# Kernel tuning notes

Hardware: AMD Instinct MI355X
Metric: run time of the kernel (lower is better)

Reference implementation:

```python
import jax, jax.numpy as jnp
import numpy as np
from jax import lax

B = 1024
T = 32           # length_sec = 384 // (2*2*3*1)
HGT = 7          # height_image = 28 // (1*2*2*1)
CC = 32          # last conv channels
AD = HGT * CC    # abstract_dim = 224
HID = 256        # attention decoder hidden
VOCAB = 29
OUT_LEN = 25


def setup_inputs() -> dict:
    ks = jax.random.split(jax.random.key(0), 24)
    n = lambda k, s, sc=1.0: jax.random.normal(k, s, jnp.float32) * sc
    return {
        "x": n(ks[0], (B, 1, 384, 28)),
        "conv1_w": n(ks[1], (4, 1, 3, 3), 0.2),   "conv1_b": n(ks[2], (4,), 0.1),
        "conv2_w": n(ks[3], (16, 4, 3, 3), 0.2),  "conv2_b": n(ks[4], (16,), 0.1),
        "conv3_w": n(ks[5], (16, 16, 3, 3), 0.2), "conv3_b": n(ks[6], (16,), 0.1),
        "conv4_w": n(ks[7], (32, 16, 3, 3), 0.2), "conv4_b": n(ks[8], (32,), 0.1),
        "h0": n(ks[9], (1, AD)), "c0": n(ks[10], (1, AD)),
        "lstm_Wih": n(ks[11], (4 * AD, AD), 0.05), "lstm_Whh": n(ks[12], (4 * AD, AD), 0.05),
        "lstm_bih": n(ks[13], (4 * AD,), 0.05),    "lstm_bhh": n(ks[14], (4 * AD,), 0.05),
        "att_w": n(ks[15], (1, HID + AD), 0.05),   "att_b": n(ks[16], (1,), 0.05),
        "dec_Wih": n(ks[17], (4 * HID, AD), 0.05), "dec_Whh": n(ks[18], (4 * HID, HID), 0.05),
        "dec_bih": n(ks[19], (4 * HID,), 0.05),    "dec_bhh": n(ks[20], (4 * HID,), 0.05),
        "out_w": n(ks[21], (VOCAB, HID), 0.05),    "out_b": n(ks[22], (VOCAB,), 0.05),
    }


def _lstm_cell(h, c, xt, Wih, Whh, bih, bhh):
    # PyTorch gate order: i, f, g, o
    g = xt @ Wih.T + bih + h @ Whh.T + bhh
    i, f, gg, o = jnp.split(g, 4, axis=-1)
    c = jax.nn.sigmoid(f) * c + jax.nn.sigmoid(i) * jnp.tanh(gg)
    h = jax.nn.sigmoid(o) * jnp.tanh(c)
    return h, c


def reference(x, conv1_w, conv1_b, conv2_w, conv2_b, conv3_w, conv3_b, conv4_w, conv4_b,
              h0, c0, lstm_Wih, lstm_Whh, lstm_bih, lstm_bhh,
              att_w, att_b, dec_Wih, dec_Whh, dec_bih, dec_bhh, out_w, out_b):
    def crp(z, w, b, pool):
        y = lax.conv_general_dilated(z, w, (1, 1), [(1, 1), (1, 1)],
                                     dimension_numbers=('NCHW', 'OIHW', 'NCHW'))
        y = jax.nn.relu(y + b[None, :, None, None])
        win = (1, 1) + pool
        return lax.reduce_window(y, -jnp.inf, lax.max, win, win, 'VALID')

    y1 = crp(x, conv1_w, conv1_b, (2, 1))
    y2 = crp(y1, conv2_w, conv2_b, (2, 2))
    y3 = crp(y2, conv3_w, conv3_b, (3, 2))
    y4 = crp(y3, conv4_w, conv4_b, (1, 1))          # [B, 32, 32, 7]
    Bsz = x.shape[0]
    # y5[b,t,i] = y4[b, i%32, t, i//32]  ==  transpose + reshape (replaces python loop)
    y5 = jnp.transpose(y4, (0, 2, 3, 1)).reshape(Bsz, T, AD)   # [B, T, 224]

    # encoder LSTM (seq-major scan, like torch LSTM)
    def estep(carry, xt):
        h, c = carry
        h, c = _lstm_cell(h, c, xt, lstm_Wih, lstm_Whh, lstm_bih, lstm_bhh)
        return (h, c), h
    h0b = jnp.tile(h0, (Bsz, 1))
    c0b = jnp.tile(c0, (Bsz, 1))
    _, hs = lax.scan(estep, (h0b, c0b), jnp.transpose(y5, (1, 0, 2)))
    y8 = jnp.transpose(hs, (1, 0, 2))                # [B, T, 224]

    # attention decoder: additive score softmax(linear(concat(h, enc)))
    w_h = att_w[0, :HID]     # hidden part
    w_e = att_w[0, HID:]     # encoder part
    enc_score = y8 @ w_e     # [B, T], precomputed once

    def dstep(carry, _):
        h, c = carry
        scores = enc_score + (h @ w_h)[:, None] + att_b[0]      # [B, T]
        alpha = jax.nn.softmax(scores, axis=1)
        ctx = jnp.einsum('bt,btd->bd', alpha, y8)               # [B, 224]
        h, c = _lstm_cell(h, c, ctx, dec_Wih, dec_Whh, dec_bih, dec_bhh)
        return (h, c), h @ out_w.T + out_b                      # [B, 29]

    hdec = jnp.zeros((Bsz, HID), x.dtype)
    _, outs = lax.scan(dstep, (hdec, hdec), None, length=OUT_LEN)  # [25, B, 29]
    return jnp.transpose(outs, (1, 2, 0))            # [B, 29, 25]
```

## Files before the change

kernel.cpp:

```cpp
#include <hip/hip_runtime.h>

typedef unsigned short u16;
typedef unsigned int u32;
typedef unsigned long long u64;
typedef __bf16 bfrag __attribute__((ext_vector_type(8)));
typedef float v4f __attribute__((ext_vector_type(4)));

#define DI __device__ __forceinline__

DI float bf2f(u16 b){ union{u32 u; float f;} c; c.u = ((u32)b)<<16; return c.f; }
DI u16 f2bf(float f){ union{float f; u32 u;} c; c.f=f; u32 u=c.u; return (u16)((u + 0x7FFFu + ((u>>16)&1u))>>16); }
DI float sigm(float x){ return 1.0f/(1.0f+__expf(-x)); }
DI float tanhf_(float x){ float a=fabsf(x); float e=__expf(2.0f*a); float r=1.0f-2.0f/(e+1.0f); return x<0.0f? -r : r; }

__global__ __launch_bounds__(256) void k_cvt2(const float* __restrict__ src, u16* __restrict__ hi,
                                              u16* __restrict__ lo, u32 n){
  u32 i = blockIdx.x*256u + threadIdx.x;
  if (i < n){ float v = src[i]; u16 h = f2bf(v); hi[i] = h; lo[i] = f2bf(v - bf2f(h)); }
}

__global__ __launch_bounds__(256) void k_conv1(const float* __restrict__ x, const float* __restrict__ w,
                                               const float* __restrict__ bias, float* __restrict__ y1q, u32 bbase){
  u32 gid = blockIdx.x*256u + threadIdx.x;
  u32 bl = gid/768u, r = gid - bl*768u;
  u32 oy = r>>2, xg = r&3u;
  const float* xb = x + (u64)(bbase+bl)*10752u;
  float win[4][9];
  #pragma unroll
  for (int rr=0; rr<4; rr++){
    int iy = 2*(int)oy - 1 + rr;
    bool vy = (u32)iy < 384u;
    #pragma unroll
    for (int cc=0; cc<9; cc++){
      int ix = (int)(xg*7u) + cc - 1;
      win[rr][cc] = (vy && (u32)ix < 28u) ? xb[iy*28 + ix] : 0.0f;
    }
  }
  #pragma unroll
  for (int co=0; co<4; co++){
    float wf[9];
    #pragma unroll
    for (int j=0;j<9;j++) wf[j] = w[co*9+j];
    float bc = bias[co];
    float* outp = y1q + ((u64)(bl*4u+co)*192u + oy)*28u + xg*7u;
    #pragma unroll
    for (int ox=0; ox<7; ox++){
      float m = 0.0f;
      #pragma unroll
      for (int py=0; py<2; py++){
        float s = bc;
        #pragma unroll
        for (int dy=0; dy<3; dy++)
          #pragma unroll
          for (int dx=0; dx<3; dx++)
            s += win[py+dy][ox+dx]*wf[dy*3+dx];
        m = fmaxf(m, s);
      }
      outp[ox] = m;
    }
  }
}

__global__ __launch_bounds__(256) void k_conv2(const float* __restrict__ y1q, const float* __restrict__ w,
                                               const float* __restrict__ bias, float* __restrict__ y2q){
  u32 gid = blockIdx.x*256u + threadIdx.x;
  u32 bl = gid/1536u, r = gid - bl*1536u;
  u32 oy = r>>4, xg = (r>>3)&1u, cp = r&7u;
  const float* inb = y1q + (u64)bl*21504u;
  float acc[2][7][4];
  #pragma unroll
  for (int c2=0;c2<2;c2++)
    #pragma unroll
    for (int i=0;i<7;i++){ acc[c2][i][0]=0.f;acc[c2][i][1]=0.f;acc[c2][i][2]=0.f;acc[c2][i][3]=0.f; }
  for (int ci=0; ci<4; ci++){
    float win[4][16];
    const float* pl = inb + ci*5376;
    #pragma unroll
    for (int rr=0; rr<4; rr++){
      int iy = 2*(int)oy - 1 + rr;
      bool vy = (u32)iy < 192u;
      #pragma unroll
      for (int cc=0; cc<16; cc++){
        int ix = (int)(xg*14u) + cc - 1;
        win[rr][cc] = (vy && (u32)ix<28u) ? pl[iy*28+ix] : 0.0f;
      }
    }
    float wf[2][9];
    #pragma unroll
    for (int c2=0;c2<2;c2++)
      #pragma unroll
      for (int j=0;j<9;j++) wf[c2][j] = w[((cp*2u+(u32)c2)*4u+(u32)ci)*9u+j];
    #pragma unroll
    for (int c2=0;c2<2;c2++)
      #pragma unroll
      for (int ol=0; ol<7; ol++)
        #pragma unroll
        for (int py=0; py<2; py++)
          #pragma unroll
          for (int px=0; px<2; px++){
            float s = acc[c2][ol][py*2+px];
            #pragma unroll
            for (int dy=0; dy<3; dy++)
              #pragma unroll
              for (int dx=0; dx<3; dx++)
                s += win[py+dy][2*ol+px+dx]*wf[c2][dy*3+dx];
            acc[c2][ol][py*2+px] = s;
          }
  }
  #pragma unroll
  for (int c2=0;c2<2;c2++){
    u32 co = cp*2u+(u32)c2;
    float bc = bias[co];
    float* outp = y2q + ((u64)(bl*16u+co)*96u + oy)*14u + xg*7u;
    #pragma unroll
    for (int ol=0; ol<7; ol++){
      float m = fmaxf(fmaxf(acc[c2][ol][0],acc[c2][ol][1]), fmaxf(acc[c2][ol][2],acc[c2][ol][3])) + bc;
      outp[ol] = fmaxf(m, 0.0f);
    }
  }
}

__global__ __launch_bounds__(256) void k_conv3(const float* __restrict__ y2q, const float* __restrict__ w,
                                               const float* __restrict__ bias, float* __restrict__ y3, u32 bbase){
  u32 gid = blockIdx.x*256u + threadIdx.x;
  u32 bl = gid/512u, r = gid - bl*512u;
  u32 oy = r>>4, co = r&15u;
  const float* inb = y2q + (u64)bl*21504u;
  float acc[7][6];
  #pragma unroll
  for (int i=0;i<7;i++){
    #pragma unroll
    for (int j=0;j<6;j++) acc[i][j]=0.0f;
  }
  for (int ci=0; ci<16; ci++){
    float win[5][16];
    const float* pl = inb + ci*1344;
    #pragma unroll
    for (int rr=0; rr<5; rr++){
      int iy = 3*(int)oy - 1 + rr;
      bool vy = (u32)iy < 96u;
      #pragma unroll
      for (int cc=0; cc<16; cc++){
        int ix = cc-1;
        win[rr][cc] = (vy && (u32)ix<14u) ? pl[iy*14+ix] : 0.0f;
      }
    }
    float wf[9];
    #pragma unroll
    for (int j=0;j<9;j++) wf[j] = w[((u32)co*16u+(u32)ci)*9u+j];
    #pragma unroll
    for (int ox=0; ox<7; ox++){
      #pragma unroll
      for (int py=0; py<3; py++)
        #pragma unroll
        for (int px=0; px<2; px++){
          float s = acc[ox][py*2+px];
          #pragma unroll
          for (int dy=0; dy<3; dy++)
            #pragma unroll
            for (int dx=0; dx<3; dx++)
              s += win[py+dy][2*ox+px+dx]*wf[dy*3+dx];
          acc[ox][py*2+px] = s;
        }
    }
  }
  float bc = bias[co];
  float* outp = y3 + ((u64)((bbase+bl)*16u+co)*32u + oy)*7u;
  #pragma unroll
  for (int ox=0; ox<7; ox++){
    float m = acc[ox][0];
    #pragma unroll
    for (int j=1;j<6;j++) m = fmaxf(m, acc[ox][j]);
    outp[ox] = fmaxf(m + bc, 0.0f);
  }
}

__global__ __launch_bounds__(256) void k_conv4(const float* __restrict__ y3, const float* __restrict__ w,
                                               const float* __restrict__ bias, float* __restrict__ y5){
  u32 gid = blockIdx.x*256u + threadIdx.x;
  u32 b = gid/512u, r = gid - b*512u;
  u32 oy = r>>4, cp = r&15u;
  u32 co0 = cp*2u;
  const float* inb = y3 + (u64)b*3584u;
  float acc[2][7];
  #pragma unroll
  for (int i=0;i<2;i++){
    #pragma unroll
    for (int j=0;j<7;j++) acc[i][j]=0.0f;
  }
  for (int ci=0; ci<16; ci++){
    float win[3][9];
    const float* pl = inb + ci*224;
    #pragma unroll
    for (int rr=0; rr<3; rr++){
      int iy = (int)oy - 1 + rr;
      bool vy = (u32)iy < 32u;
      #pragma unroll
      for (int cc=0; cc<9; cc++){
        int ix = cc-1;
        win[rr][cc] = (vy && (u32)ix<7u) ? pl[iy*7+ix] : 0.0f;
      }
    }
    #pragma unroll
    for (int c2=0; c2<2; c2++){
      float wf[9];
      #pragma unroll
      for (int j=0;j<9;j++) wf[j] = w[((co0+(u32)c2)*16u+(u32)ci)*9u+j];
      #pragma unroll
      for (int ox=0; ox<7; ox++){
        float s = acc[c2][ox];
        #pragma unroll
        for (int dy=0; dy<3; dy++)
          #pragma unroll
          for (int dx=0; dx<3; dx++)
            s += win[dy][ox+dx]*wf[dy*3+dx];
        acc[c2][ox] = s;
      }
    }
  }
  #pragma unroll
  for (int c2=0; c2<2; c2++){
    float bc = bias[co0+(u32)c2];
    #pragma unroll
    for (int ox=0; ox<7; ox++)
      y5[((u64)b*32u + oy)*224u + (u32)ox*32u + (co0+(u32)c2)] = fmaxf(acc[c2][ox] + bc, 0.0f);
  }
}

__global__ __launch_bounds__(1024) void k_zero(u32* __restrict__ p){
  p[threadIdx.x] = 0u;
}

__global__ __launch_bounds__(512, 4) void k_enc7(const u16* __restrict__ WihHi, const u16* __restrict__ WihLo,
                                                 const u16* __restrict__ WhhHi, const u16* __restrict__ WhhLo,
                                                 const float* __restrict__ bih, const float* __restrict__ bhh,
                                                 const float* __restrict__ y5, const float* __restrict__ h0,
                                                 const float* __restrict__ c0, float* __restrict__ y8,
                                                 u32* __restrict__ eflags){
  __shared__ __align__(16) u16 Ahi[16*456], Alo[16*456];
  __shared__ __align__(16) float gsh[16*132];
  __shared__ __align__(16) float bsh[128];
  u32 tid = threadIdx.x, w = tid>>6, lane = tid&63u, nl = lane&15u, quad = lane>>4;
  u32 bid = blockIdx.x, g = bid & 63u, q = bid >> 6;
  u32 b0 = g*16u, hc0 = q*32u;
  if (tid < 128u){
    u32 gi = tid>>5, col = gi*224u + hc0 + (tid&31u);
    bsh[tid] = bih[col] + bhh[col];
  }
  for (u32 it=tid; it<3584u; it+=512u){
    u32 r = it/224u, c = it - r*224u;
    float v = h0[c]; u16 hb = f2bf(v);
    Ahi[r*456u+224u+c] = hb; Alo[r*456u+224u+c] = f2bf(v - bf2f(hb));
  }
  float creg = c0[hc0 + (tid&31u)];
  u32* fE = eflags + g*16u;
  const u32 col = (w>>1)*224u + hc0 + (w&1u)*16u + nl;
  const u32 gl  = (w>>1)*32u  + (w&1u)*16u + nl;
  __syncthreads();
  for (u32 t=0; t<32u; t++){
    #pragma unroll
    for (int i=0;i<7;i++){
      u32 item = (u32)i*512u + tid;
      u32 r = item/224u, c = item - r*224u;
      float v = y5[((u64)(b0+r)*32u + t)*224u + c];
      u16 hb = f2bf(v);
      Ahi[r*456u+c] = hb; Alo[r*456u+c] = f2bf(v - bf2f(hb));
    }
    __syncthreads();
    v4f acc = {};
    #pragma unroll
    for (int kt=0; kt<14; kt++){
      u32 ka = (u32)kt*32u + quad*8u;
      bfrag ah = *(const bfrag*)&Ahi[nl*456u + ka];
      bfrag al = *(const bfrag*)&Alo[nl*456u + ka];
      bfrag bh, bl;
      if (kt<7){
        u64 o = (u64)col*224u + ka;
        bh = *(const bfrag*)&WihHi[o]; bl = *(const bfrag*)&WihLo[o];
      } else {
        u64 o = (u64)col*224u + (ka - 224u);
        bh = *(const bfrag*)&WhhHi[o]; bl = *(const bfrag*)&WhhLo[o];
      }
      acc = __builtin_amdgcn_mfma_f32_16x16x32_bf16(ah, bh, acc, 0,0,0);
      acc = __builtin_amdgcn_mfma_f32_16x16x32_bf16(al, bh, acc, 0,0,0);
      acc = __builtin_amdgcn_mfma_f32_16x16x32_bf16(ah, bl, acc, 0,0,0);
    }
    #pragma unroll
    for (int rg=0; rg<4; rg++)
      gsh[(quad*4u+(u32)rg)*132u + gl] = acc[rg];
    __syncthreads();
    {
      u32 row = tid>>5, hl = tid&31u;
      float gi_ = gsh[row*132u +       hl] + bsh[hl];
      float gf_ = gsh[row*132u + 32u + hl] + bsh[32u+hl];
      float gg_ = gsh[row*132u + 64u + hl] + bsh[64u+hl];
      float go_ = gsh[row*132u + 96u + hl] + bsh[96u+hl];
      float cv = sigm(gf_)*creg + sigm(gi_)*tanhf_(gg_);
      float hv = sigm(go_)*tanhf_(cv);
      creg = cv;
      union{float f; u32 u;} cu; cu.f = hv;
      __hip_atomic_store((u32*)&y8[((u64)(b0+row)*32u + t)*224u + hc0 + hl], cu.u,
                         __ATOMIC_RELAXED, __HIP_MEMORY_SCOPE_AGENT);
    }
    __syncthreads();
    if (tid==0u)
      __hip_atomic_fetch_add(fE, 1u, __ATOMIC_RELEASE, __HIP_MEMORY_SCOPE_AGENT);
    if (t < 31u){
      if (tid==0u){
        while (__hip_atomic_load(fE, __ATOMIC_RELAXED, __HIP_MEMORY_SCOPE_AGENT) < 7u*(t+1u))
          __builtin_amdgcn_s_sleep(2);
      }
      __syncthreads();
      for (u32 it=tid; it<3584u; it+=512u){
        u32 r = it/224u, c = it - r*224u;
        u32 uv = __hip_atomic_load((const u32*)&y8[((u64)(b0+r)*32u + t)*224u + c],
                                   __ATOMIC_RELAXED, __HIP_MEMORY_SCOPE_AGENT);
        union{u32 u; float f;} cu; cu.u = uv;
        u16 hb = f2bf(cu.f);
        Ahi[r*456u+224u+c] = hb; Alo[r*456u+224u+c] = f2bf(cu.f - bf2f(hb));
      }
    }
  }
}

__global__ __launch_bounds__(512, 2) void k_dec4(const float* __restrict__ y8,
    const float* __restrict__ attw, const float* __restrict__ attb,
    const u16* __restrict__ WihHi, const u16* __restrict__ WihLo,
    const u16* __restrict__ WhhHi, const u16* __restrict__ WhhLo,
    const float* __restrict__ bih, const float* __restrict__ bhh,
    u32* __restrict__ hist, u32* __restrict__ ctxc, u32* __restrict__ flags){
  __shared__ __align__(16) u16 Ahi[16*488], Alo[16*488];
  __shared__ __align__(16) float ysl[28672];
  __shared__ __align__(16) float ugsh[16*257];
  float* gshv = ugsh;
  float* alpv = ugsh;
  u32 tid=threadIdx.x, w=tid>>6, lane=tid&63u, nl=lane&15u, quad=lane>>4;
  u32 p = blockIdx.x, xcd = p&7u, slot = p>>3;
  u32 q = xcd>>1;
  u32 g = (xcd&1u)*32u + slot;
  u32 b0 = g*16u, hc0 = q*64u;
  float breg[4];
  #pragma unroll
  for (int gi2=0; gi2<4; gi2++){
    u32 colb = (u32)gi2*256u + hc0 + (tid&63u);
    breg[gi2] = bih[colb] + bhh[colb];
  }
  for (u32 it=tid; it<4096u; it+=512u){
    u32 r=it>>8, c=it&255u;
    Ahi[r*488u+224u+c]=0; Alo[r*488u+224u+c]=0;
  }
  float escr;
  {
    u32 r=tid>>5, t=tid&31u;
    const float* yr = y8 + ((u64)(b0+r)*32u + t)*224u;
    const float* we = attw + 256;
    float sacc=0.0f;
    #pragma unroll 8
    for (int j=0;j<224;j++) sacc += yr[j]*we[j];
    escr = sacc + attb[0];
  }
  for (u32 it2=tid; it2<28672u; it2+=512u){
    u32 tt = it2/896u, rem = it2 - tt*896u;
    u32 rr = rem/56u, ccl = rem - rr*56u;
    ysl[it2] = y8[(u64)(b0+rr)*7168u + tt*224u + q*56u + ccl];
  }
  const u32 rrA = tid/56u, ccA = tid - rrA*56u + q*56u;
  const u32 itB = tid + 512u;
  const u32 rrB = itB/56u, ccB = itB - rrB*56u + q*56u;
  float cst[2] = {0.0f, 0.0f};
  u32* fh = flags + g*16u;
  u32* fc = flags + g*16u + 8u;
  const u32 nt0 = w, nt1 = w + 8u;
  const u32 col0 = (nt0>>2)*256u + hc0 + (nt0&3u)*16u + nl;
  const u32 col1 = (nt1>>2)*256u + hc0 + (nt1&3u)*16u + nl;
  const u32 gl0  = (nt0>>2)*64u + (nt0&3u)*16u + nl;
  const u32 gl1  = (nt1>>2)*64u + (nt1&3u)*16u + nl;
  __syncthreads();
  for (u32 s=0; s<25u; s++){
    if (s>0u){
      if (tid==0u){
        while (__hip_atomic_load(fh, __ATOMIC_RELAXED, __HIP_MEMORY_SCOPE_AGENT) < 4u*s)
          __builtin_amdgcn_s_sleep(2);
      }
      __syncthreads();
      u32* hrow = hist + ((u64)(s-1u)*1024u + b0)*256u;
      for (u32 it=tid; it<4096u; it+=512u){
        u32 v = __hip_atomic_load(&hrow[it], __ATOMIC_RELAXED, __HIP_MEMORY_SCOPE_AGENT);
        u32 r = it>>8, c = it&255u;
        Ahi[r*488u+224u+c] = (u16)(v>>16); Alo[r*488u+224u+c] = (u16)(v&0xFFFFu);
      }
      __syncthreads();
    }
    {
      u32 r=tid>>5, t=tid&31u;
      float part=0.0f;
      if (s>0u){
        #pragma unroll
        for (int qq=0; qq<8; qq++){
          u32 c = t + (u32)qq*32u;
          float hvf = bf2f(Ahi[r*488u+224u+c]) + bf2f(Alo[r*488u+224u+c]);
          part += hvf*attw[c];
        }
        #pragma unroll
        for (int off=16; off; off>>=1) part += __shfl_xor(part, off, 32);
      }
      float sv = escr + part;
      float mx = sv;
      #pragma unroll
      for (int off=16; off; off>>=1) mx = fmaxf(mx, __shfl_xor(mx, off, 32));
      float e = __expf(sv-mx);
      float ssum = e;
      #pragma unroll
      for (int off=16; off; off>>=1) ssum += __shfl_xor(ssum, off, 32);
      alpv[r*32u+t] = e/ssum;
    }
    __syncthreads();
    u32* cdst = ctxc + (u64)(s&1u)*229376u + (u64)g*3584u;
    {
      float a0=0.0f;
      #pragma unroll
      for (int tt=0; tt<32; tt++) a0 += alpv[rrA*32u+(u32)tt]*ysl[(u32)tt*896u + tid];
      u16 hb = f2bf(a0), lb = f2bf(a0 - bf2f(hb));
      __hip_atomic_store(&cdst[rrA*224u+ccA], ((u32)hb<<16)|(u32)lb, __ATOMIC_RELAXED, __HIP_MEMORY_SCOPE_AGENT);
      if (tid < 384u){
        float a1=0.0f;
        #pragma unroll
        for (int tt=0; tt<32; tt++) a1 += alpv[rrB*32u+(u32)tt]*ysl[(u32)tt*896u + itB];
        u16 hb1 = f2bf(a1), lb1 = f2bf(a1 - bf2f(hb1));
        __hip_atomic_store(&cdst[rrB*224u+ccB], ((u32)hb1<<16)|(u32)lb1, __ATOMIC_RELAXED, __HIP_MEMORY_SCOPE_AGENT);
      }
    }
    __syncthreads();
    if (tid==0u){
      __hip_atomic_fetch_add(fc, 1u, __ATOMIC_RELEASE, __HIP_MEMORY_SCOPE_AGENT);
      while (__hip_atomic_load(fc, __ATOMIC_RELAXED, __HIP_MEMORY_SCOPE_AGENT) < 4u*(s+1u))
        __builtin_amdgcn_s_sleep(2);
    }
    __syncthreads();
    for (u32 it=tid; it<3584u; it+=512u){
      u32 v = __hip_atomic_load(&cdst[it], __ATOMIC_RELAXED, __HIP_MEMORY_SCOPE_AGENT);
      u32 rr = it/224u, cc = it - rr*224u;
      Ahi[rr*488u+cc] = (u16)(v>>16); Alo[rr*488u+cc] = (u16)(v&0xFFFFu);
    }
    __syncthreads();
    v4f acc0 = {}, acc1 = {};
    #pragma unroll
    for (int kt=0; kt<15; kt++){
      u32 ka = (u32)kt*32u + quad*8u;
      bfrag afh = *(const bfrag*)&Ahi[nl*488u + ka];
      bfrag afl = *(const bfrag*)&Alo[nl*488u + ka];
      bfrag b0h, b0l, b1h, b1l;
      if (kt<7){
        u64 o0 = (u64)col0*224u + ka, o1 = (u64)col1*224u + ka;
        b0h = *(const bfrag*)&WihHi[o0]; b0l = *(const bfrag*)&WihLo[o0];
        b1h = *(const bfrag*)&WihHi[o1]; b1l = *(const bfrag*)&WihLo[o1];
      } else {
        u32 kb = ka - 224u;
        u64 o0 = (u64)col0*256u + kb, o1 = (u64)col1*256u + kb;
        b0h = *(const bfrag*)&WhhHi[o0]; b0l = *(const bfrag*)&WhhLo[o0];
        b1h = *(const bfrag*)&WhhHi[o1]; b1l = *(const bfrag*)&WhhLo[o1];
      }
      acc0 = __builtin_amdgcn_mfma_f32_16x16x32_bf16(afh, b0h, acc0, 0,0,0);
      acc0 = __builtin_amdgcn_mfma_f32_16x16x32_bf16(afl, b0h, acc0, 0,0,0);
      acc0 = __builtin_amdgcn_mfma_f32_16x16x32_bf16(afh, b0l, acc0, 0,0,0);
      acc1 = __builtin_amdgcn_mfma_f32_16x16x32_bf16(afh, b1h, acc1, 0,0,0);
      acc1 = __builtin_amdgcn_mfma_f32_16x16x32_bf16(afl, b1h, acc1, 0,0,0);
      acc1 = __builtin_amdgcn_mfma_f32_16x16x32_bf16(afh, b1l, acc1, 0,0,0);
    }
    #pragma unroll
    for (int rg=0; rg<4; rg++){
      gshv[(quad*4u+(u32)rg)*257u + gl0] = acc0[rg];
      gshv[(quad*4u+(u32)rg)*257u + gl1] = acc1[rg];
    }
    __syncthreads();
    u32* hdst = hist + ((u64)s*1024u + b0)*256u + hc0;
    #pragma unroll
    for (int k2=0; k2<2; k2++){
      u32 l = (u32)k2*512u + tid;
      u32 row = l>>6, hl = l&63u;
      float gi_ = gshv[row*257u + hl]         + breg[0];
      float gf_ = gshv[row*257u + 64u  + hl]  + breg[1];
      float gg_ = gshv[row*257u + 128u + hl]  + breg[2];
      float go_ = gshv[row*257u + 192u + hl]  + breg[3];
      float cv = sigm(gf_)*cst[k2] + sigm(gi_)*tanhf_(gg_);
      float hv = sigm(go_)*tanhf_(cv);
      cst[k2] = cv;
      u16 hb = f2bf(hv), lb = f2bf(hv - bf2f(hb));
      __hip_atomic_store(&hdst[row*256u + hl], ((u32)hb<<16)|(u32)lb, __ATOMIC_RELAXED, __HIP_MEMORY_SCOPE_AGENT);
    }
    __syncthreads();
    if (tid==0u)
      __hip_atomic_fetch_add(fh, 1u, __ATOMIC_RELEASE, __HIP_MEMORY_SCOPE_AGENT);
  }
}

__global__ __launch_bounds__(256) void k_out(const u32* __restrict__ hist, const float* __restrict__ outw,
                                             const float* __restrict__ outb, float* __restrict__ outp){
  __shared__ __align__(16) float wsh[29*260];
  __shared__ __align__(16) float hrow[256];
  u32 tid = threadIdx.x, b = blockIdx.x;
  for (u32 it=tid; it<7424u; it+=256u){
    u32 v = it/256u, c = it&255u;
    wsh[v*260u+c] = outw[v*256u+c];
  }
  __syncthreads();
  for (u32 s=0; s<25u; s++){
    u32 v = hist[((u64)s*1024u + b)*256u + tid];
    hrow[tid] = bf2f((u16)(v>>16)) + bf2f((u16)(v&0xFFFFu));
    __syncthreads();
    if (tid < 232u){
      u32 vv = tid>>3, k8 = tid&7u;
      float a = 0.0f;
      #pragma unroll
      for (int j=0;j<32;j++) a += hrow[k8*32u+(u32)j]*wsh[vv*260u + k8*32u + (u32)j];
      #pragma unroll
      for (int off=4; off; off>>=1) a += __shfl_xor(a, off, 8);
      if (k8==0u) outp[((u64)b*29u + vv)*25u + s] = a + outb[vv];
    }
    __syncthreads();
  }
}

extern "C" void kernel_launch(void* const* d_in, const int* in_sizes, int n_in,
                              void* d_out, int out_size, void* d_ws, size_t ws_size,
                              hipStream_t stream){
  (void)in_sizes; (void)n_in; (void)out_size; (void)ws_size;
  const float* x    = (const float*)d_in[0];
  const float* c1w  = (const float*)d_in[1];
  const float* c1b  = (const float*)d_in[2];
  const float* c2w  = (const float*)d_in[3];
  const float* c2b  = (const float*)d_in[4];
  const float* c3w  = (const float*)d_in[5];
  const float* c3b  = (const float*)d_in[6];
  const float* c4w  = (const float*)d_in[7];
  const float* c4b  = (const float*)d_in[8];
  const float* h0   = (const float*)d_in[9];
  const float* c0   = (const float*)d_in[10];
  const float* lWih = (const float*)d_in[11];
  const float* lWhh = (const float*)d_in[12];
  const float* lbih = (const float*)d_in[13];
  const float* lbhh = (const float*)d_in[14];
  const float* attw = (const float*)d_in[15];
  const float* attb = (const float*)d_in[16];
  const float* dWih = (const float*)d_in[17];
  const float* dWhh = (const float*)d_in[18];
  const float* dbih = (const float*)d_in[19];
  const float* dbhh = (const float*)d_in[20];
  const float* outw = (const float*)d_in[21];
  const float* outb = (const float*)d_in[22];
  float* out = (float*)d_out;
  char* ws = (char*)d_ws;
  float* y1q = (float*)(ws);
  float* y2q = (float*)(ws + 22020096ull);
  float* y3  = (float*)(ws + 44040192ull);
  float* y5  = (float*)(ws);
  float* y8  = (float*)(ws + 29360128ull);
  u32* hist  = (u32*)(ws);
  u32* ctxc  = (u32*)(ws + 26214400ull);
  u32* flags = (u32*)(ws + 28049408ull);
  u16* lWihHi = (u16*)(ws + 58720256ull);
  u16* lWihLo = (u16*)(ws + 59121664ull);
  u16* lWhhHi = (u16*)(ws + 59523072ull);
  u16* lWhhLo = (u16*)(ws + 59924480ull);
  u16* dWihHi = (u16*)(ws + 60325888ull);
  u16* dWihLo = (u16*)(ws + 60784640ull);
  u16* dWhhHi = (u16*)(ws + 61243392ull);
  u16* dWhhLo = (u16*)(ws + 61767680ull);
  u32* eflags = (u32*)d_out;

  k_cvt2<<<dim3(784),  dim3(256), 0, stream>>>(lWih, lWihHi, lWihLo, 200704u);
  k_cvt2<<<dim3(784),  dim3(256), 0, stream>>>(lWhh, lWhhHi, lWhhLo, 200704u);
  k_cvt2<<<dim3(896),  dim3(256), 0, stream>>>(dWih, dWihHi, dWihLo, 229376u);
  k_cvt2<<<dim3(1024), dim3(256), 0, stream>>>(dWhh, dWhhHi, dWhhLo, 262144u);
  for (u32 q=0; q<4; q++){
    k_conv1<<<dim3(768),  dim3(256), 0, stream>>>(x, c1w, c1b, y1q, q*256u);
    k_conv2<<<dim3(1536), dim3(256), 0, stream>>>(y1q, c2w, c2b, y2q);
    k_conv3<<<dim3(512),  dim3(256), 0, stream>>>(y2q, c3w, c3b, y3, q*256u);
  }
  k_conv4<<<dim3(2048), dim3(256), 0, stream>>>(y3, c4w, c4b, y5);
  k_zero <<<dim3(1), dim3(1024), 0, stream>>>(eflags);
  k_enc7 <<<dim3(448), dim3(512), 0, stream>>>(lWihHi, lWihLo, lWhhHi, lWhhLo, lbih, lbhh,
                                               y5, h0, c0, y8, eflags);
  k_zero <<<dim3(1), dim3(1024), 0, stream>>>(flags);
  k_dec4 <<<dim3(256), dim3(512), 0, stream>>>(y8, attw, attb, dWihHi, dWihLo, dWhhHi, dWhhLo,
                                               dbih, dbhh, hist, ctxc, flags);
  k_out  <<<dim3(1024), dim3(256), 0, stream>>>(hist, outw, outb, out);
}
```

Baseline: 2.059 ms.

## Make decoder blocks self-contained with 4 batch rows each, removing cross-block flags

The decoder used to split each group of 16 batch rows across 4 blocks by hidden-column quarter. Those blocks exchanged context vectors and hidden states through global memory, with atomic flag spin-waits every step. Now each block owns 4 batch rows and computes all 1024 gate columns itself, keeping h and ctx in shared memory and only writing hist for the output kernel. This removes inter-block synchronisation and global round-trips. In exchange, each block streams the full decoder weight matrices every step, uses MFMA tiles only a quarter full (4 of 16 rows), and does 4x more weight traffic overall.

After: 4.361 ms. 2.12x slower.

```diff
diff --git a/kernel.cpp b/kernel.cpp
--- a/kernel.cpp
+++ b/kernel.cpp
@@ -323,75 +323,47 @@
   }
 }
 
-__global__ __launch_bounds__(512, 2) void k_dec4(const float* __restrict__ y8,
+__global__ __launch_bounds__(512, 2) void k_dec1(const float* __restrict__ y8,
     const float* __restrict__ attw, const float* __restrict__ attb,
     const u16* __restrict__ WihHi, const u16* __restrict__ WihLo,
     const u16* __restrict__ WhhHi, const u16* __restrict__ WhhLo,
     const float* __restrict__ bih, const float* __restrict__ bhh,
-    u32* __restrict__ hist, u32* __restrict__ ctxc, u32* __restrict__ flags){
-  __shared__ __align__(16) u16 Ahi[16*488], Alo[16*488];
+    u32* __restrict__ hist){
   __shared__ __align__(16) float ysl[28672];
-  __shared__ __align__(16) float ugsh[16*257];
-  float* gshv = ugsh;
-  float* alpv = ugsh;
-  u32 tid=threadIdx.x, w=tid>>6, lane=tid&63u, nl=lane&15u, quad=lane>>4;
-  u32 p = blockIdx.x, xcd = p&7u, slot = p>>3;
-  u32 q = xcd>>1;
-  u32 g = (xcd&1u)*32u + slot;
-  u32 b0 = g*16u, hc0 = q*64u;
-  float breg[4];
-  #pragma unroll
-  for (int gi2=0; gi2<4; gi2++){
-    u32 colb = (u32)gi2*256u + hc0 + (tid&63u);
-    breg[gi2] = bih[colb] + bhh[colb];
-  }
-  for (u32 it=tid; it<4096u; it+=512u){
+  __shared__ __align__(16) u16 Ahi[4*488], Alo[4*488];
+  __shared__ __align__(16) float gshq[4*1028];
+  __shared__ __align__(16) float alp[132];
+  u32 tid = threadIdx.x, w = tid>>6, lane = tid&63u, nl = lane&15u, quad = lane>>4;
+  u32 b0 = blockIdx.x*4u;
+  for (u32 it=tid; it<28672u; it+=512u){
+    u32 t = it/896u, rem = it - t*896u;
+    u32 r = rem/224u, c = rem - r*224u;
+    ysl[it] = y8[((u64)(b0+r)*32u + t)*224u + c];
+  }
+  for (u32 it=tid; it<1024u; it+=512u){
     u32 r=it>>8, c=it&255u;
     Ahi[r*488u+224u+c]=0; Alo[r*488u+224u+c]=0;
   }
-  float escr;
+  float breg[4];
   {
+    u32 hl8 = tid&255u;
+    #pragma unroll
+    for (int gi2=0; gi2<4; gi2++)
+      breg[gi2] = bih[(u32)gi2*256u + hl8] + bhh[(u32)gi2*256u + hl8];
+  }
+  __syncthreads();
+  float escr = 0.0f;
+  if (tid < 128u){
     u32 r=tid>>5, t=tid&31u;
-    const float* yr = y8 + ((u64)(b0+r)*32u + t)*224u;
     const float* we = attw + 256;
     float sacc=0.0f;
     #pragma unroll 8
-    for (int j=0;j<224;j++) sacc += yr[j]*we[j];
+    for (int j=0;j<224;j++) sacc += ysl[t*896u + r*224u + (u32)j]*we[j];
     escr = sacc + attb[0];
   }
-  for (u32 it2=tid; it2<28672u; it2+=512u){
-    u32 tt = it2/896u, rem = it2 - tt*896u;
-    u32 rr = rem/56u, ccl = rem - rr*56u;
-    ysl[it2] = y8[(u64)(b0+rr)*7168u + tt*224u + q*56u + ccl];
-  }
-  const u32 rrA = tid/56u, ccA = tid - rrA*56u + q*56u;
-  const u32 itB = tid + 512u;
-  const u32 rrB = itB/56u, ccB = itB - rrB*56u + q*56u;
   float cst[2] = {0.0f, 0.0f};
-  u32* fh = flags + g*16u;
-  u32* fc = flags + g*16u + 8u;
-  const u32 nt0 = w, nt1 = w + 8u;
-  const u32 col0 = (nt0>>2)*256u + hc0 + (nt0&3u)*16u + nl;
-  const u32 col1 = (nt1>>2)*256u + hc0 + (nt1&3u)*16u + nl;
-  const u32 gl0  = (nt0>>2)*64u + (nt0&3u)*16u + nl;
-  const u32 gl1  = (nt1>>2)*64u + (nt1&3u)*16u + nl;
-  __syncthreads();
   for (u32 s=0; s<25u; s++){
-    if (s>0u){
-      if (tid==0u){
-        while (__hip_atomic_load(fh, __ATOMIC_RELAXED, __HIP_MEMORY_SCOPE_AGENT) < 4u*s)
-          __builtin_amdgcn_s_sleep(2);
-      }
-      __syncthreads();
-      u32* hrow = hist + ((u64)(s-1u)*1024u + b0)*256u;
-      for (u32 it=tid; it<4096u; it+=512u){
-        u32 v = __hip_atomic_load(&hrow[it], __ATOMIC_RELAXED, __HIP_MEMORY_SCOPE_AGENT);
-        u32 r = it>>8, c = it&255u;
-        Ahi[r*488u+224u+c] = (u16)(v>>16); Alo[r*488u+224u+c] = (u16)(v&0xFFFFu);
-      }
-      __syncthreads();
-    }
-    {
+    if (tid < 128u){
       u32 r=tid>>5, t=tid&31u;
       float part=0.0f;
       if (s>0u){
@@ -412,85 +384,73 @@
       float ssum = e;
       #pragma unroll
       for (int off=16; off; off>>=1) ssum += __shfl_xor(ssum, off, 32);
-      alpv[r*32u+t] = e/ssum;
-    }
-    __syncthreads();
-    u32* cdst = ctxc + (u64)(s&1u)*229376u + (u64)g*3584u;
+      alp[(tid>>5)*32u + (tid&31u)] = e/ssum;
+    }
+    __syncthreads();
     {
+      u32 r = tid/224u, c = tid - r*224u;
       float a0=0.0f;
       #pragma unroll
-      for (int tt=0; tt<32; tt++) a0 += alpv[rrA*32u+(u32)tt]*ysl[(u32)tt*896u + tid];
-      u16 hb = f2bf(a0), lb = f2bf(a0 - bf2f(hb));
-      __hip_atomic_store(&cdst[rrA*224u+ccA], ((u32)hb<<16)|(u32)lb, __ATOMIC_RELAXED, __HIP_MEMORY_SCOPE_AGENT);
+      for (int tt=0; tt<32; tt++) a0 += alp[r*32u+(u32)tt]*ysl[(u32)tt*896u + tid];
+      u16 hb = f2bf(a0);
+      Ahi[r*488u+c] = hb; Alo[r*488u+c] = f2bf(a0 - bf2f(hb));
       if (tid < 384u){
+        u32 it2 = tid + 512u;
+        u32 r2 = it2/224u, c2 = it2 - r2*224u;
         float a1=0.0f;
         #pragma unroll
-        for (int tt=0; tt<32; tt++) a1 += alpv[rrB*32u+(u32)tt]*ysl[(u32)tt*896u + itB];
-        u16 hb1 = f2bf(a1), lb1 = f2bf(a1 - bf2f(hb1));
-        __hip_atomic_store(&cdst[rrB*224u+ccB], ((u32)hb1<<16)|(u32)lb1, __ATOMIC_RELAXED, __HIP_MEMORY_SCOPE_AGENT);
-      }
-    }
-    __syncthreads();
-    if (tid==0u){
-      __hip_atomic_fetch_add(fc, 1u, __ATOMIC_RELEASE, __HIP_MEMORY_SCOPE_AGENT);
-      while (__hip_atomic_load(fc, __ATOMIC_RELAXED, __HIP_MEMORY_SCOPE_AGENT) < 4u*(s+1u))
-        __builtin_amdgcn_s_sleep(2);
-    }
-    __syncthreads();
-    for (u32 it=tid; it<3584u; it+=512u){
-      u32 v = __hip_atomic_load(&cdst[it], __ATOMIC_RELAXED, __HIP_MEMORY_SCOPE_AGENT);
-      u32 rr = it/224u, cc = it - rr*224u;
-      Ahi[rr*488u+cc] = (u16)(v>>16); Alo[rr*488u+cc] = (u16)(v&0xFFFFu);
-    }
-    __syncthreads();
-    v4f acc0 = {}, acc1 = {};
+        for (int tt=0; tt<32; tt++) a1 += alp[r2*32u+(u32)tt]*ysl[(u32)tt*896u + it2];
+        u16 hb1 = f2bf(a1);
+        Ahi[r2*488u+c2] = hb1; Alo[r2*488u+c2] = f2bf(a1 - bf2f(hb1));
+      }
+    }
+    __syncthreads();
+    v4f acc[8] = {};
     #pragma unroll
     for (int kt=0; kt<15; kt++){
       u32 ka = (u32)kt*32u + quad*8u;
-      bfrag afh = *(const bfrag*)&Ahi[nl*488u + ka];
-      bfrag afl = *(const bfrag*)&Alo[nl*488u + ka];
-      bfrag b0h, b0l, b1h, b1l;
-      if (kt<7){
-        u64 o0 = (u64)col0*224u + ka, o1 = (u64)col1*224u + ka;
-        b0h = *(const bfrag*)&WihHi[o0]; b0l = *(const bfrag*)&WihLo[o0];
-        b1h = *(const bfrag*)&WihHi[o1]; b1l = *(const bfrag*)&WihLo[o1];
-      } else {
-        u32 kb = ka - 224u;
-        u64 o0 = (u64)col0*256u + kb, o1 = (u64)col1*256u + kb;
-        b0h = *(const bfrag*)&WhhHi[o0]; b0l = *(const bfrag*)&WhhLo[o0];
-        b1h = *(const bfrag*)&WhhHi[o1]; b1l = *(const bfrag*)&WhhLo[o1];
-      }
-      acc0 = __builtin_amdgcn_mfma_f32_16x16x32_bf16(afh, b0h, acc0, 0,0,0);
-      acc0 = __builtin_amdgcn_mfma_f32_16x16x32_bf16(afl, b0h, acc0, 0,0,0);
-      acc0 = __builtin_amdgcn_mfma_f32_16x16x32_bf16(afh, b0l, acc0, 0,0,0);
-      acc1 = __builtin_amdgcn_mfma_f32_16x16x32_bf16(afh, b1h, acc1, 0,0,0);
-      acc1 = __builtin_amdgcn_mfma_f32_16x16x32_bf16(afl, b1h, acc1, 0,0,0);
-      acc1 = __builtin_amdgcn_mfma_f32_16x16x32_bf16(afh, b1l, acc1, 0,0,0);
-    }
-    #pragma unroll
-    for (int rg=0; rg<4; rg++){
-      gshv[(quad*4u+(u32)rg)*257u + gl0] = acc0[rg];
-      gshv[(quad*4u+(u32)rg)*257u + gl1] = acc1[rg];
-    }
-    __syncthreads();
-    u32* hdst = hist + ((u64)s*1024u + b0)*256u + hc0;
+      bfrag afh = *(const bfrag*)&Ahi[(nl&3u)*488u + ka];
+      bfrag afl = *(const bfrag*)&Alo[(nl&3u)*488u + ka];
+      #pragma unroll
+      for (int j=0; j<8; j++){
+        u32 col = (w*8u + (u32)j)*16u + nl;
+        bfrag bh, bl;
+        if (kt<7){
+          u64 o = (u64)col*224u + ka;
+          bh = *(const bfrag*)&WihHi[o]; bl = *(const bfrag*)&WihLo[o];
+        } else {
+          u64 o = (u64)col*256u + (ka - 224u);
+          bh = *(const bfrag*)&WhhHi[o]; bl = *(const bfrag*)&WhhLo[o];
+        }
+        acc[j] = __builtin_amdgcn_mfma_f32_16x16x32_bf16(afh, bh, acc[j], 0,0,0);
+        acc[j] = __builtin_amdgcn_mfma_f32_16x16x32_bf16(afl, bh, acc[j], 0,0,0);
+        acc[j] = __builtin_amdgcn_mfma_f32_16x16x32_bf16(afh, bl, acc[j], 0,0,0);
+      }
+    }
+    if (quad == 0u){
+      #pragma unroll
+      for (int j=0; j<8; j++)
+        #pragma unroll
+        for (int rg=0; rg<4; rg++)
+          gshq[(u32)rg*1028u + (w*8u+(u32)j)*16u + nl] = acc[j][rg];
+    }
+    __syncthreads();
     #pragma unroll
     for (int k2=0; k2<2; k2++){
       u32 l = (u32)k2*512u + tid;
-      u32 row = l>>6, hl = l&63u;
-      float gi_ = gshv[row*257u + hl]         + breg[0];
-      float gf_ = gshv[row*257u + 64u  + hl]  + breg[1];
-      float gg_ = gshv[row*257u + 128u + hl]  + breg[2];
-      float go_ = gshv[row*257u + 192u + hl]  + breg[3];
+      u32 row = l>>8, hl = l&255u;
+      float gi_ = gshq[row*1028u +        hl] + breg[0];
+      float gf_ = gshq[row*1028u + 256u + hl] + breg[1];
+      float gg_ = gshq[row*1028u + 512u + hl] + breg[2];
+      float go_ = gshq[row*1028u + 768u + hl] + breg[3];
       float cv = sigm(gf_)*cst[k2] + sigm(gi_)*tanhf_(gg_);
       float hv = sigm(go_)*tanhf_(cv);
       cst[k2] = cv;
       u16 hb = f2bf(hv), lb = f2bf(hv - bf2f(hb));
-      __hip_atomic_store(&hdst[row*256u + hl], ((u32)hb<<16)|(u32)lb, __ATOMIC_RELAXED, __HIP_MEMORY_SCOPE_AGENT);
-    }
-    __syncthreads();
-    if (tid==0u)
-      __hip_atomic_fetch_add(fh, 1u, __ATOMIC_RELEASE, __HIP_MEMORY_SCOPE_AGENT);
+      Ahi[row*488u+224u+hl] = hb; Alo[row*488u+224u+hl] = lb;
+      hist[((u64)s*1024u + b0 + row)*256u + hl] = ((u32)hb<<16)|(u32)lb;
+    }
+    __syncthreads();
   }
 }
 
@@ -556,8 +516,6 @@
   float* y5  = (float*)(ws);
   float* y8  = (float*)(ws + 29360128ull);
   u32* hist  = (u32*)(ws);
-  u32* ctxc  = (u32*)(ws + 26214400ull);
-  u32* flags = (u32*)(ws + 28049408ull);
   u16* lWihHi = (u16*)(ws + 58720256ull);
   u16* lWihLo = (u16*)(ws + 59121664ull);
   u16* lWhhHi = (u16*)(ws + 59523072ull);
@@ -581,8 +539,7 @@
   k_zero <<<dim3(1), dim3(1024), 0, stream>>>(eflags);
   k_enc7 <<<dim3(448), dim3(512), 0, stream>>>(lWihHi, lWihLo, lWhhHi, lWhhLo, lbih, lbhh,
                                                y5, h0, c0, y8, eflags);
-  k_zero <<<dim3(1), dim3(1024), 0, stream>>>(flags);
-  k_dec4 <<<dim3(256), dim3(512), 0, stream>>>(y8, attw, attb, dWihHi, dWihLo, dWhhHi, dWhhLo,
-                                               dbih, dbhh, hist, ctxc, flags);
+  k_dec1 <<<dim3(256), dim3(512), 0, stream>>>(y8, attw, attb, dWihHi, dWihLo, dWhhHi, dWhhLo,
+                                               dbih, dbhh, hist);
   k_out  <<<dim3(1024), dim3(256), 0, stream>>>(hist, outw, outb, out);
 }
```
